# Kernel optimization log

Measured on AMD Instinct MI355X. Metric: run time of the kernel, lower is better.

## Reference

```python
import jax, jax.numpy as jnp
import numpy as np

B, S, IN_DIM = 16, 1024, 64
D, H, FF, L, OUT = 512, 8, 2048, 6, 256
HD = D // H
EPS = 1e-5


def _ln(x, g, b):
    m = jnp.mean(x, axis=-1, keepdims=True)
    v = jnp.var(x, axis=-1, keepdims=True)
    return (x - m) * jax.lax.rsqrt(v + EPS) * g + b


def setup_inputs() -> dict:
    key = jax.random.key(0)
    ks = jax.random.split(key, 24)
    def rn(k, shape, scale=0.02):
        return jax.random.normal(k, shape, dtype=jnp.float32) * scale
    return {
        "x": jax.random.normal(ks[0], (B, S, IN_DIM), dtype=jnp.float32),
        "in_w": rn(ks[1], (IN_DIM, D)), "in_b": jnp.zeros((D,), jnp.float32),
        "in_ln_g": jnp.ones((D,), jnp.float32), "in_ln_b": jnp.zeros((D,), jnp.float32),
        "pos": rn(ks[2], (S, D)),
        "qkv_w": rn(ks[3], (L, D, 3 * D)), "qkv_b": jnp.zeros((L, 3 * D), jnp.float32),
        "ao_w": rn(ks[4], (L, D, D)), "ao_b": jnp.zeros((L, D), jnp.float32),
        "ff_w1": rn(ks[5], (L, D, FF)), "ff_b1": jnp.zeros((L, FF), jnp.float32),
        "ff_w2": rn(ks[6], (L, FF, D)), "ff_b2": jnp.zeros((L, D), jnp.float32),
        "ln1_g": jnp.ones((L, D), jnp.float32), "ln1_b": jnp.zeros((L, D), jnp.float32),
        "ln2_g": jnp.ones((L, D), jnp.float32), "ln2_b": jnp.zeros((L, D), jnp.float32),
        "o_w1": rn(ks[7], (D, D // 2)), "o_b1": jnp.zeros((D // 2,), jnp.float32),
        "o_ln_g": jnp.ones((D // 2,), jnp.float32), "o_ln_b": jnp.zeros((D // 2,), jnp.float32),
        "o_w2": rn(ks[8], (D // 2, OUT)), "o_b2": jnp.zeros((OUT,), jnp.float32),
    }


def reference(x, in_w, in_b, in_ln_g, in_ln_b, pos,
              qkv_w, qkv_b, ao_w, ao_b, ff_w1, ff_b1, ff_w2, ff_b2,
              ln1_g, ln1_b, ln2_g, ln2_b,
              o_w1, o_b1, o_ln_g, o_ln_b, o_w2, o_b2):
    h = x @ in_w + in_b                      # [B,S,D]
    h = _ln(h, in_ln_g, in_ln_b)
    h = h + pos[None, :, :]
    scale = 1.0 / jnp.sqrt(jnp.float32(HD))
    for l in range(L):
        qkv = h @ qkv_w[l] + qkv_b[l]        # [B,S,3D]
        q, k, v = jnp.split(qkv, 3, axis=-1)
        q = q.reshape(B, S, H, HD)
        k = k.reshape(B, S, H, HD)
        v = v.reshape(B, S, H, HD)
        scores = jnp.einsum('bqhd,bkhd->bhqk', q, k) * scale
        attn = jax.nn.softmax(scores, axis=-1)
        ctx = jnp.einsum('bhqk,bkhd->bqhd', attn, v).reshape(B, S, D)
        attn_out = ctx @ ao_w[l] + ao_b[l]
        h = _ln(h + attn_out, ln1_g[l], ln1_b[l])
        ff = jax.nn.gelu(h @ ff_w1[l] + ff_b1[l], approximate=False) @ ff_w2[l] + ff_b2[l]
        h = _ln(h + ff, ln2_g[l], ln2_b[l])
    pooled = jnp.mean(h, axis=1)             # [B,D]
    z = jax.nn.gelu(pooled @ o_w1 + o_b1, approximate=False)
    z = _ln(z, o_ln_g, o_ln_b)
    return z @ o_w2 + o_b2                   # [B,OUT]
```

## Files before the change

kernel.cpp:

```cpp
#include <hip/hip_runtime.h>
#include <hip/hip_bf16.h>

#define B_ 16
#define S_ 1024
#define IN_ 64
#define D_ 512
#define H_ 8
#define HD_ 64
#define FF_ 2048
#define L_ 6
#define OUT_ 256
#define BS_ (B_*S_)

typedef __attribute__((ext_vector_type(8))) short s16x8;
typedef __attribute__((ext_vector_type(4))) short s16x4;
typedef __attribute__((ext_vector_type(4))) float f32x4;

#define AS1(p) ((const __attribute__((address_space(1))) void*)(p))
#define AS3(p) ((__attribute__((address_space(3))) void*)(p))

__device__ __forceinline__ ushort f2bf(float x) {
  __hip_bfloat16 h = __float2bfloat16(x);
  return *reinterpret_cast<ushort*>(&h);
}
__device__ __forceinline__ float bf2f(ushort u) {
  unsigned v = ((unsigned)u) << 16;
  union { unsigned u; float f; } c; c.u = v; return c.f;
}
__device__ __forceinline__ float gelu_exact(float x) {
  return 0.5f * x * (1.0f + erff(x * 0.70710678118654752f));
}

template<int BN, int WM, int WN, int MODE>
__global__ __launch_bounds__(256)
void gemm_bt(const ushort* __restrict__ A, int lda,
             const ushort* __restrict__ Bt, int ldb,
             const float* __restrict__ bias,
             ushort* __restrict__ C, int ldc,
             int K)
{
  constexpr int BM = 128;
  constexpr int BK = 64;
  constexpr int FM = BM / (WM * 16);
  constexpr int FN = BN / (WN * 16);
  constexpr int CP = 136;
  __shared__ union {
    struct { ushort a[BM * BK]; ushort b[BN * BK]; } s;
    ushort c[BM * CP];
  } u;

  const int tid = threadIdx.x;
  const int lane = tid & 63;
  const int wave = tid >> 6;
  const int wr = wave / WN;
  const int wc = wave % WN;
  const int lrow = lane & 15;
  const int lk = (lane >> 4) * 8;

  const int gx = gridDim.x;
  const int nwg = gx * gridDim.y;
  const int flat = blockIdx.y * gx + blockIdx.x;
  const int T = (flat & 7) * (nwg >> 3) + (flat >> 3);
  const int m0 = (T / gx) * BM;
  const int n0 = (T % gx) * BN;

  f32x4 acc[FM][FN];
#pragma unroll
  for (int m = 0; m < FM; ++m)
#pragma unroll
    for (int n = 0; n < FN; ++n)
      acc[m][n] = (f32x4){0.f, 0.f, 0.f, 0.f};

  for (int k0 = 0; k0 < K; k0 += BK) {
    __syncthreads();
#pragma unroll
    for (int rr = 0; rr < BM / 32; ++rr) {
      int c = rr * 256 + tid;
      int row = c >> 3, cg = c & 7;
      __builtin_amdgcn_global_load_lds(
          AS1(A + (size_t)(m0 + row) * lda + k0 + cg * 8),
          AS3(u.s.a + (size_t)(rr * 256 + wave * 64) * 8), 16, 0, 0);
    }
#pragma unroll
    for (int rr = 0; rr < BN / 32; ++rr) {
      int c = rr * 256 + tid;
      int row = c >> 3, cg = c & 7;
      __builtin_amdgcn_global_load_lds(
          AS1(Bt + (size_t)(n0 + row) * ldb + k0 + cg * 8),
          AS3(u.s.b + (size_t)(rr * 256 + wave * 64) * 8), 16, 0, 0);
    }
    __syncthreads();
#pragma unroll
    for (int kk = 0; kk < 2; ++kk) {
      s16x8 a[FM], b[FN];
#pragma unroll
      for (int m = 0; m < FM; ++m)
        a[m] = *(const s16x8*)&u.s.a[(wr * FM * 16 + m * 16 + lrow) * BK + kk * 32 + lk];
#pragma unroll
      for (int n = 0; n < FN; ++n)
        b[n] = *(const s16x8*)&u.s.b[(wc * FN * 16 + n * 16 + lrow) * BK + kk * 32 + lk];
#pragma unroll
      for (int m = 0; m < FM; ++m)
#pragma unroll
        for (int n = 0; n < FN; ++n)
          acc[m][n] = __builtin_amdgcn_mfma_f32_16x16x32_bf16(a[m], b[n], acc[m][n], 0, 0, 0);
    }
  }

  __syncthreads();
  const int rbL = wr * FM * 16 + (lane >> 4) * 4;
  const int cbL = wc * FN * 16 + lrow;
#pragma unroll
  for (int n = 0; n < FN; ++n) {
    int colL = cbL + n * 16;
    float bv = bias ? bias[n0 + colL] : 0.0f;
#pragma unroll
    for (int m = 0; m < FM; ++m) {
#pragma unroll
      for (int r = 0; r < 4; ++r) {
        float v = acc[m][n][r] + bv;
        if (MODE == 2) v = gelu_exact(v);
        u.c[(rbL + m * 16 + r) * CP + colL] = f2bf(v);
      }
    }
  }
  __syncthreads();
  if (MODE == 3) {
    int dl = tid >> 1, kh = tid & 1;
    int vcol = n0 + dl;
    int bb = m0 >> 10, k0r = m0 & 1023;
    ushort* vrow = C + ((size_t)(bb * 8 + (vcol >> 6)) * HD_ + (vcol & 63)) * S_
                   + k0r + kh * 64;
#pragma unroll
    for (int w2 = 0; w2 < 2; ++w2)
#pragma unroll
      for (int g2 = 0; g2 < 4; ++g2) {
        ushort outv[8];
#pragma unroll
        for (int jj = 0; jj < 8; ++jj) {
          int pk = kh * 64 + w2 * 32 + (jj < 4 ? 4 * g2 + jj : 16 + 4 * g2 + (jj - 4));
          outv[jj] = u.c[pk * CP + dl];
        }
        *(s16x8*)(vrow + w2 * 32 + g2 * 8) = *(s16x8*)outv;
      }
  } else {
#pragma unroll
    for (int p = 0; p < 8; ++p) {
      int row = p * 16 + (tid >> 4);
      int col = (tid & 15) * 8;
      s16x8 v = *(const s16x8*)&u.c[row * CP + col];
      *(s16x8*)&C[(size_t)(m0 + row) * ldc + n0 + col] = v;
    }
  }
}

__global__ __launch_bounds__(512)
void flash_kernel(const ushort* __restrict__ qkv, const ushort* __restrict__ vt,
                  ushort* __restrict__ ctx)
{
  constexpr int KB = 128;
  const float KE = 0.125f * 1.44269504f;
  __shared__ ushort ks[KB][72];
  __shared__ ushort vs[HD_][KB + 8];
  const int tid = threadIdx.x;
  const int lane = tid & 63;
  const int wave = tid >> 6;
  const int lrow = lane & 15;
  const int g = lane >> 4;
  const int lk = g * 8;

  const int flat = blockIdx.y * 8 + blockIdx.x;
  const int T = (flat & 7) * 128 + (flat >> 3);
  const int bh = T >> 3;
  const int b = bh >> 3, h = bh & 7;
  const int q0 = (T & 7) * 128;

  s16x8 qf[2];
  {
    const ushort* qrow = qkv + ((size_t)(b * S_ + q0 + wave * 16 + lrow)) * (3 * D_) + h * HD_;
    s16x8 r0 = *(const s16x8*)(qrow + lk);
    s16x8 r1 = *(const s16x8*)(qrow + 32 + lk);
#pragma unroll
    for (int j = 0; j < 8; ++j) {
      qf[0][j] = (short)f2bf(bf2f((ushort)r0[j]) * KE);
      qf[1][j] = (short)f2bf(bf2f((ushort)r1[j]) * KE);
    }
  }
  float lsum = 0.f;
  f32x4 o[4] = {};

  for (int kt = 0; kt < S_ / KB; ++kt) {
    __syncthreads();
    for (int c = tid; c < KB * 8; c += 512) {
      int row = c >> 3, cg = c & 7;
      *(s16x8*)&ks[row][cg * 8] =
          *(const s16x8*)(qkv + ((size_t)(b * S_ + kt * KB + row)) * (3 * D_) + D_ + h * HD_ + cg * 8);
    }
    for (int c = tid; c < HD_ * 16; c += 512) {
      int row = c >> 4, cg = c & 15;
      *(s16x8*)&vs[row][cg * 8] =
          *(const s16x8*)(vt + ((size_t)(bh * HD_ + row)) * S_ + kt * KB + cg * 8);
    }
    __syncthreads();

#pragma unroll
    for (int tp = 0; tp < 4; ++tp) {
      f32x4 s0 = {}, s1 = {};
      {
        s16x8 k00 = *(const s16x8*)&ks[tp * 32 + lrow][lk];
        s16x8 k01 = *(const s16x8*)&ks[tp * 32 + lrow][32 + lk];
        s16x8 k10 = *(const s16x8*)&ks[tp * 32 + 16 + lrow][lk];
        s16x8 k11 = *(const s16x8*)&ks[tp * 32 + 16 + lrow][32 + lk];
        s0 = __builtin_amdgcn_mfma_f32_16x16x32_bf16(k00, qf[0], s0, 0, 0, 0);
        s0 = __builtin_amdgcn_mfma_f32_16x16x32_bf16(k01, qf[1], s0, 0, 0, 0);
        s1 = __builtin_amdgcn_mfma_f32_16x16x32_bf16(k10, qf[0], s1, 0, 0, 0);
        s1 = __builtin_amdgcn_mfma_f32_16x16x32_bf16(k11, qf[1], s1, 0, 0, 0);
      }
      union { s16x8 v; unsigned u[4]; } pa;
      {
        float p0 = exp2f(s0[0]), p1 = exp2f(s0[1]);
        float p2 = exp2f(s0[2]), p3 = exp2f(s0[3]);
        float p4 = exp2f(s1[0]), p5 = exp2f(s1[1]);
        float p6 = exp2f(s1[2]), p7 = exp2f(s1[3]);
        lsum += ((p0 + p1) + (p2 + p3)) + ((p4 + p5) + (p6 + p7));
        unsigned u0 = __float_as_uint(p0) + 0x8000u, u1 = __float_as_uint(p1) + 0x8000u;
        unsigned u2 = __float_as_uint(p2) + 0x8000u, u3 = __float_as_uint(p3) + 0x8000u;
        unsigned u4 = __float_as_uint(p4) + 0x8000u, u5 = __float_as_uint(p5) + 0x8000u;
        unsigned u6 = __float_as_uint(p6) + 0x8000u, u7 = __float_as_uint(p7) + 0x8000u;
        pa.u[0] = (u0 >> 16) | (u1 & 0xffff0000u);
        pa.u[1] = (u2 >> 16) | (u3 & 0xffff0000u);
        pa.u[2] = (u4 >> 16) | (u5 & 0xffff0000u);
        pa.u[3] = (u6 >> 16) | (u7 & 0xffff0000u);
      }
#pragma unroll
      for (int n2 = 0; n2 < 4; ++n2) {
        s16x8 vf = *(const s16x8*)&vs[n2 * 16 + lrow][tp * 32 + lk];
        o[n2] = __builtin_amdgcn_mfma_f32_16x16x32_bf16(vf, pa.v, o[n2], 0, 0, 0);
      }
    }
  }
  lsum += __shfl_xor(lsum, 16);
  lsum += __shfl_xor(lsum, 32);
  float inv = 1.0f / lsum;

  ushort* crow = ctx + ((size_t)(b * S_ + q0 + wave * 16 + lrow)) * D_ + h * HD_;
#pragma unroll
  for (int n2 = 0; n2 < 4; ++n2) {
    s16x4 w;
#pragma unroll
    for (int r = 0; r < 4; ++r) w[r] = (short)f2bf(o[n2][r] * inv);
    *(s16x4*)(crow + n2 * 16 + g * 4) = w;
  }
}

__global__ __launch_bounds__(256)
void ln512_kernel(const ushort* __restrict__ a, const ushort* __restrict__ res,
                  const float* __restrict__ g, const float* __restrict__ bt,
                  const float* __restrict__ pos,
                  ushort* __restrict__ hout)
{
  const int row = blockIdx.x;
  const int t = threadIdx.x;
  const size_t base = (size_t)row * D_;
  float x0 = bf2f(a[base + t]), x1 = bf2f(a[base + t + 256]);
  if (res) { x0 += bf2f(res[base + t]); x1 += bf2f(res[base + t + 256]); }
  float s = x0 + x1, q = x0 * x0 + x1 * x1;
#pragma unroll
  for (int m = 32; m > 0; m >>= 1) { s += __shfl_xor(s, m); q += __shfl_xor(q, m); }
  __shared__ float red[8];
  if ((t & 63) == 0) { red[(t >> 6) * 2] = s; red[(t >> 6) * 2 + 1] = q; }
  __syncthreads();
  s = red[0] + red[2] + red[4] + red[6];
  q = red[1] + red[3] + red[5] + red[7];
  float mean = s * (1.0f / D_);
  float var = q * (1.0f / D_) - mean * mean;
  float rs = rsqrtf(var + 1e-5f);
  float y0 = (x0 - mean) * rs * g[t] + bt[t];
  float y1 = (x1 - mean) * rs * g[t + 256] + bt[t + 256];
  if (pos) {
    int sp = row & (S_ - 1);
    y0 += pos[(size_t)sp * D_ + t];
    y1 += pos[(size_t)sp * D_ + t + 256];
  }
  hout[base + t] = f2bf(y0);
  hout[base + t + 256] = f2bf(y1);
}

__global__ void wtrans_kernel(const float* __restrict__ W, ushort* __restrict__ Wt, int K, int N)
{
  __shared__ float tile[32][33];
  const float* Wl = W + (size_t)blockIdx.z * K * N;
  ushort* Wtl = Wt + (size_t)blockIdx.z * K * N;
  int n0 = blockIdx.x * 32, k0 = blockIdx.y * 32;
  int tx = threadIdx.x, ty = threadIdx.y;
#pragma unroll
  for (int r = 0; r < 4; ++r)
    tile[ty * 4 + r][tx] = Wl[(size_t)(k0 + ty * 4 + r) * N + n0 + tx];
  __syncthreads();
#pragma unroll
  for (int r = 0; r < 4; ++r)
    Wtl[(size_t)(n0 + ty * 4 + r) * K + k0 + tx] = f2bf(tile[tx][ty * 4 + r]);
}

__global__ void castx_kernel(const float* __restrict__ x, ushort* __restrict__ xb, int n)
{
  int i = blockIdx.x * blockDim.x + threadIdx.x;
  if (i < n) xb[i] = f2bf(x[i]);
}

__global__ __launch_bounds__(256)
void pool_partial_kernel(const ushort* __restrict__ h, float* __restrict__ pp)
{
  int b = blockIdx.x, ch = blockIdx.y;
  int t = threadIdx.x;
  float s0 = 0, s1 = 0;
  for (int r = 0; r < 128; ++r) {
    size_t base = ((size_t)b * S_ + ch * 128 + r) * D_;
    s0 += bf2f(h[base + t]);
    s1 += bf2f(h[base + t + 256]);
  }
  pp[(size_t)(b * 8 + ch) * D_ + t] = s0;
  pp[(size_t)(b * 8 + ch) * D_ + t + 256] = s1;
}

__global__ __launch_bounds__(256)
void head_kernel(const float* __restrict__ pp,
                 const float* __restrict__ w1, const float* __restrict__ b1,
                 const float* __restrict__ lg, const float* __restrict__ lb,
                 const float* __restrict__ w2, const float* __restrict__ b2,
                 float* __restrict__ out)
{
  __shared__ float pooled[D_];
  __shared__ float z[256];
  int b = blockIdx.x, t = threadIdx.x;
  for (int i = t; i < D_; i += 256) {
    float s = 0;
    for (int c = 0; c < 8; ++c) s += pp[(size_t)(b * 8 + c) * D_ + i];
    pooled[i] = s * (1.0f / S_);
  }
  __syncthreads();
  float acc = 0;
  for (int k = 0; k < D_; ++k) acc += pooled[k] * w1[(size_t)k * 256 + t];
  float zz = gelu_exact(acc + b1[t]);
  float s = zz, q = zz * zz;
#pragma unroll
  for (int m = 32; m > 0; m >>= 1) { s += __shfl_xor(s, m); q += __shfl_xor(q, m); }
  __shared__ float red[8];
  if ((t & 63) == 0) { red[(t >> 6) * 2] = s; red[(t >> 6) * 2 + 1] = q; }
  __syncthreads();
  s = red[0] + red[2] + red[4] + red[6];
  q = red[1] + red[3] + red[5] + red[7];
  float mean = s * (1.0f / 256), var = q * (1.0f / 256) - mean * mean;
  float rs = rsqrtf(var + 1e-5f);
  z[t] = (zz - mean) * rs * lg[t] + lb[t];
  __syncthreads();
  float o = 0;
  for (int k = 0; k < 256; ++k) o += z[k] * w2[(size_t)k * 256 + t];
  out[(size_t)b * 256 + t] = o + b2[t];
}

extern "C" void kernel_launch(void* const* d_in, const int* in_sizes, int n_in,
                              void* d_out, int out_size, void* d_ws, size_t ws_size,
                              hipStream_t stream)
{
  const float* x       = (const float*)d_in[0];
  const float* in_w    = (const float*)d_in[1];
  const float* in_b    = (const float*)d_in[2];
  const float* in_ln_g = (const float*)d_in[3];
  const float* in_ln_b = (const float*)d_in[4];
  const float* pos     = (const float*)d_in[5];
  const float* qkv_w   = (const float*)d_in[6];
  const float* qkv_b   = (const float*)d_in[7];
  const float* ao_w    = (const float*)d_in[8];
  const float* ao_b    = (const float*)d_in[9];
  const float* ff_w1   = (const float*)d_in[10];
  const float* ff_b1   = (const float*)d_in[11];
  const float* ff_w2   = (const float*)d_in[12];
  const float* ff_b2   = (const float*)d_in[13];
  const float* ln1_g   = (const float*)d_in[14];
  const float* ln1_b   = (const float*)d_in[15];
  const float* ln2_g   = (const float*)d_in[16];
  const float* ln2_b   = (const float*)d_in[17];
  const float* o_w1    = (const float*)d_in[18];
  const float* o_b1    = (const float*)d_in[19];
  const float* o_ln_g  = (const float*)d_in[20];
  const float* o_ln_b  = (const float*)d_in[21];
  const float* o_w2    = (const float*)d_in[22];
  const float* o_b2    = (const float*)d_in[23];

  char* wp = (char*)d_ws;
  auto alloc = [&](size_t bytes) {
    char* p = wp;
    wp += (bytes + 255) & ~(size_t)255;
    return p;
  };
  ushort* hb     = (ushort*)alloc((size_t)BS_ * D_ * 2);
  ushort* tmpb   = (ushort*)alloc((size_t)BS_ * D_ * 2);
  ushort* big    = (ushort*)alloc((size_t)BS_ * FF_ * 2);
  ushort* ctxb   = (ushort*)alloc((size_t)BS_ * D_ * 2);
  ushort* xb     = (ushort*)alloc((size_t)BS_ * IN_ * 2);
  ushort* vt     = (ushort*)alloc((size_t)B_ * H_ * HD_ * S_ * 2);
  float*  pp     = (float*) alloc((size_t)B_ * 8 * D_ * 4);
  ushort* in_wt  = (ushort*)alloc((size_t)D_ * IN_ * 2);
  ushort* qkv_wt = (ushort*)alloc((size_t)L_ * 3 * D_ * D_ * 2);
  ushort* ao_wt  = (ushort*)alloc((size_t)L_ * D_ * D_ * 2);
  ushort* ff1_wt = (ushort*)alloc((size_t)L_ * FF_ * D_ * 2);
  ushort* ff2_wt = (ushort*)alloc((size_t)L_ * D_ * FF_ * 2);
  (void)ws_size; (void)n_in; (void)in_sizes; (void)out_size;

  dim3 wb(32, 8);
  wtrans_kernel<<<dim3(D_ / 32, IN_ / 32, 1), wb, 0, stream>>>(in_w, in_wt, IN_, D_);
  wtrans_kernel<<<dim3(3 * D_ / 32, D_ / 32, L_), wb, 0, stream>>>(qkv_w, qkv_wt, D_, 3 * D_);
  wtrans_kernel<<<dim3(D_ / 32, D_ / 32, L_), wb, 0, stream>>>(ao_w, ao_wt, D_, D_);
  wtrans_kernel<<<dim3(FF_ / 32, D_ / 32, L_), wb, 0, stream>>>(ff_w1, ff1_wt, D_, FF_);
  wtrans_kernel<<<dim3(D_ / 32, FF_ / 32, L_), wb, 0, stream>>>(ff_w2, ff2_wt, FF_, D_);
  castx_kernel<<<BS_ * IN_ / 256, 256, 0, stream>>>(x, xb, BS_ * IN_);

  gemm_bt<128, 2, 2, 1><<<dim3(D_ / 128, BS_ / 128), 256, 0, stream>>>(
      xb, IN_, in_wt, IN_, in_b, tmpb, D_, IN_);
  ln512_kernel<<<BS_, 256, 0, stream>>>(tmpb, nullptr, in_ln_g, in_ln_b, pos, hb);

  for (int l = 0; l < L_; ++l) {
    const ushort* qwt = qkv_wt + (size_t)l * 3 * D_ * D_;
    const float*  qb  = qkv_b + (size_t)l * 3 * D_;
    gemm_bt<128, 2, 2, 1><<<dim3(2 * D_ / 128, BS_ / 128), 256, 0, stream>>>(
        hb, D_, qwt, D_, qb, big, 3 * D_, D_);
    gemm_bt<128, 2, 2, 3><<<dim3(D_ / 128, BS_ / 128), 256, 0, stream>>>(
        hb, D_, qwt + (size_t)(2 * D_) * D_, D_, qb + 2 * D_, vt, S_, D_);
    flash_kernel<<<dim3(S_ / 128, B_ * H_), 512, 0, stream>>>(big, vt, ctxb);
    gemm_bt<128, 2, 2, 1><<<dim3(D_ / 128, BS_ / 128), 256, 0, stream>>>(
        ctxb, D_, ao_wt + (size_t)l * D_ * D_, D_, ao_b + (size_t)l * D_,
        tmpb, D_, D_);
    ln512_kernel<<<BS_, 256, 0, stream>>>(tmpb, hb, ln1_g + (size_t)l * D_,
                                          ln1_b + (size_t)l * D_, nullptr, hb);
    gemm_bt<128, 2, 2, 2><<<dim3(FF_ / 128, BS_ / 128), 256, 0, stream>>>(
        hb, D_, ff1_wt + (size_t)l * FF_ * D_, D_, ff_b1 + (size_t)l * FF_,
        big, FF_, D_);
    gemm_bt<128, 2, 2, 1><<<dim3(D_ / 128, BS_ / 128), 256, 0, stream>>>(
        big, FF_, ff2_wt + (size_t)l * D_ * FF_, FF_, ff_b2 + (size_t)l * D_,
        tmpb, D_, FF_);
    ln512_kernel<<<BS_, 256, 0, stream>>>(tmpb, hb, ln2_g + (size_t)l * D_,
                                          ln2_b + (size_t)l * D_, nullptr, hb);
  }
  pool_partial_kernel<<<dim3(B_, 8), 256, 0, stream>>>(hb, pp);
  head_kernel<<<B_, 256, 0, stream>>>(pp, o_w1, o_b1, o_ln_g, o_ln_b, o_w2, o_b2,
                                      (float*)d_out);
}
```

Measured before the change: 1.830 ms.

## Double-buffer GEMM LDS tiles with async prefetch of next K slice

Restructures the GEMM main loop so that the next K tile is loaded into a second LDS buffer while MFMAs run on the current one, using vmcnt waits and raw barriers. BK is halved to 32 so that two buffers fit in the same LDS union. The aim is to hide global-to-LDS latency. The cost is twice as many barriers per unit of K. The code also assumes BN equals 128, since the staging loop hardcodes two iterations for B.

New measurement: 1.669 ms. -8.8%, faster.

```diff
diff --git a/kernel.cpp b/kernel.cpp
--- a/kernel.cpp
+++ b/kernel.cpp
@@ -40,12 +40,12 @@
              int K)
 {
   constexpr int BM = 128;
-  constexpr int BK = 64;
+  constexpr int BK = 32;
   constexpr int FM = BM / (WM * 16);
   constexpr int FN = BN / (WN * 16);
   constexpr int CP = 136;
   __shared__ union {
-    struct { ushort a[BM * BK]; ushort b[BN * BK]; } s;
+    ushort ab[2][2][BM * BK];
     ushort c[BM * CP];
   } u;
 
@@ -64,6 +64,25 @@
   const int m0 = (T / gx) * BM;
   const int n0 = (T % gx) * BN;
 
+  auto stage = [&](int bi, int k0) {
+#pragma unroll
+    for (int rr = 0; rr < 2; ++rr) {
+      int c = rr * 256 + tid;
+      int row = c >> 2, cg = c & 3;
+      __builtin_amdgcn_global_load_lds(
+          AS1(A + (size_t)(m0 + row) * lda + k0 + cg * 8),
+          AS3(u.ab[bi][0] + (size_t)(rr * 256 + wave * 64) * 8), 16, 0, 0);
+    }
+#pragma unroll
+    for (int rr = 0; rr < 2; ++rr) {
+      int c = rr * 256 + tid;
+      int row = c >> 2, cg = c & 3;
+      __builtin_amdgcn_global_load_lds(
+          AS1(Bt + (size_t)(n0 + row) * ldb + k0 + cg * 8),
+          AS3(u.ab[bi][1] + (size_t)(rr * 256 + wave * 64) * 8), 16, 0, 0);
+    }
+  };
+
   f32x4 acc[FM][FN];
 #pragma unroll
   for (int m = 0; m < FM; ++m)
@@ -71,40 +90,34 @@
     for (int n = 0; n < FN; ++n)
       acc[m][n] = (f32x4){0.f, 0.f, 0.f, 0.f};
 
-  for (int k0 = 0; k0 < K; k0 += BK) {
-    __syncthreads();
-#pragma unroll
-    for (int rr = 0; rr < BM / 32; ++rr) {
-      int c = rr * 256 + tid;
-      int row = c >> 3, cg = c & 7;
-      __builtin_amdgcn_global_load_lds(
-          AS1(A + (size_t)(m0 + row) * lda + k0 + cg * 8),
-          AS3(u.s.a + (size_t)(rr * 256 + wave * 64) * 8), 16, 0, 0);
-    }
-#pragma unroll
-    for (int rr = 0; rr < BN / 32; ++rr) {
-      int c = rr * 256 + tid;
-      int row = c >> 3, cg = c & 7;
-      __builtin_amdgcn_global_load_lds(
-          AS1(Bt + (size_t)(n0 + row) * ldb + k0 + cg * 8),
-          AS3(u.s.b + (size_t)(rr * 256 + wave * 64) * 8), 16, 0, 0);
-    }
-    __syncthreads();
-#pragma unroll
-    for (int kk = 0; kk < 2; ++kk) {
-      s16x8 a[FM], b[FN];
-#pragma unroll
-      for (int m = 0; m < FM; ++m)
-        a[m] = *(const s16x8*)&u.s.a[(wr * FM * 16 + m * 16 + lrow) * BK + kk * 32 + lk];
+  const int nt = K / BK;
+  stage(0, 0);
+  for (int t = 0; t < nt; ++t) {
+    const int cur = t & 1;
+    if (t + 1 < nt) {
+      stage(cur ^ 1, (t + 1) * BK);
+      asm volatile("s_waitcnt vmcnt(4)" ::: "memory");
+    } else {
+      asm volatile("s_waitcnt vmcnt(0)" ::: "memory");
+    }
+    __builtin_amdgcn_s_barrier();
+    __builtin_amdgcn_sched_barrier(0);
+    const ushort* Ac = u.ab[cur][0];
+    const ushort* Bc = u.ab[cur][1];
+    s16x8 a[FM], b[FN];
+#pragma unroll
+    for (int m = 0; m < FM; ++m)
+      a[m] = *(const s16x8*)&Ac[(wr * FM * 16 + m * 16 + lrow) * BK + lk];
+#pragma unroll
+    for (int n = 0; n < FN; ++n)
+      b[n] = *(const s16x8*)&Bc[(wc * FN * 16 + n * 16 + lrow) * BK + lk];
+#pragma unroll
+    for (int m = 0; m < FM; ++m)
 #pragma unroll
       for (int n = 0; n < FN; ++n)
-        b[n] = *(const s16x8*)&u.s.b[(wc * FN * 16 + n * 16 + lrow) * BK + kk * 32 + lk];
-#pragma unroll
-      for (int m = 0; m < FM; ++m)
-#pragma unroll
-        for (int n = 0; n < FN; ++n)
-          acc[m][n] = __builtin_amdgcn_mfma_f32_16x16x32_bf16(a[m], b[n], acc[m][n], 0, 0, 0);
-    }
+        acc[m][n] = __builtin_amdgcn_mfma_f32_16x16x32_bf16(a[m], b[n], acc[m][n], 0, 0, 0);
+    __builtin_amdgcn_sched_barrier(0);
+    __builtin_amdgcn_s_barrier();
   }
 
   __syncthreads();
```
